# Kernel tuning notes

Hardware: AMD Instinct MI355X
Metric: run time of the kernel (lower is better)

The kernel has to match this reference:

```python
import jax, jax.numpy as jnp
import numpy as np

B, S, H, L, OUT = 16, 64, 512, 2, 10  # batch, seq, hidden(=input_dim), num_layers, output_dim
NSTEP, TSTEP = 2, 4
L2 = L * L  # stacked LSTM layers per level_step


def setup_inputs() -> dict:
    key = jax.random.key(0)
    ks = jax.random.split(key, 24)
    s = 1.0 / np.sqrt(H)
    inp = {
        "x": jax.random.normal(ks[0], (B, S, H), jnp.float32),
        "Wp_in": jax.random.normal(ks[1], (H, H), jnp.float32) * s,
        "bp_in": jnp.zeros((H,), jnp.float32),
        "low_Wih": jax.random.normal(ks[2], (L2, 4 * H, H), jnp.float32) * s,
        "low_Whh": jax.random.normal(ks[3], (L2, 4 * H, H), jnp.float32) * s,
        "low_bih": jax.random.normal(ks[4], (L2, 4 * H), jnp.float32) * s,
        "low_bhh": jax.random.normal(ks[5], (L2, 4 * H), jnp.float32) * s,
        "high_Wih": jax.random.normal(ks[6], (L2, 4 * H, H), jnp.float32) * s,
        "high_Whh": jax.random.normal(ks[7], (L2, 4 * H, H), jnp.float32) * s,
        "high_bih": jax.random.normal(ks[8], (L2, 4 * H), jnp.float32) * s,
        "high_bhh": jax.random.normal(ks[9], (L2, 4 * H), jnp.float32) * s,
        "W_lowproj": jax.random.normal(ks[10], (H, H), jnp.float32) * s,
        "W_highproj": jax.random.normal(ks[11], (H, H), jnp.float32) * s,
        "ln_g": jnp.ones((2 * H,), jnp.float32),
        "ln_b": jnp.zeros((2 * H,), jnp.float32),
        "W1": jax.random.normal(ks[12], (H, 2 * H), jnp.float32) * (1.0 / np.sqrt(2 * H)),
        "b1": jnp.zeros((H,), jnp.float32),
        "W2": jax.random.normal(ks[13], (H // 2, H), jnp.float32) * s,
        "b2": jnp.zeros((H // 2,), jnp.float32),
        "W3": jax.random.normal(ks[14], (OUT, H // 2), jnp.float32) * (1.0 / np.sqrt(H // 2)),
        "b3": jnp.zeros((OUT,), jnp.float32),
    }
    return inp


def _lstm_layer(x, Wih, Whh, bih, bhh):
    # x: (B, S, H) -> (B, S, H), PyTorch LSTM gate order i,f,g,o, zero init state
    b, _, h = x.shape
    h0 = jnp.zeros((b, h), x.dtype)
    bias = bih + bhh

    def step(carry, xt):
        hp, cp = carry
        g = xt @ Wih.T + hp @ Whh.T + bias
        i, f, gg, o = jnp.split(g, 4, axis=-1)
        c = jax.nn.sigmoid(f) * cp + jax.nn.sigmoid(i) * jnp.tanh(gg)
        hn = jax.nn.sigmoid(o) * jnp.tanh(c)
        return (hn, c), hn

    _, ys = jax.lax.scan(step, (h0, h0), jnp.swapaxes(x, 0, 1))
    return jnp.swapaxes(ys, 0, 1)


def _run_net(x, Wih, Whh, bih, bhh):
    for l in range(Wih.shape[0]):
        x = _lstm_layer(x, Wih[l], Whh[l], bih[l], bhh[l])
    return x


def _level_step(first, second, emb, Wih, Whh, bih, bhh, Wproj):
    combined = first + second @ Wproj.T + emb  # broadcast (B,1,H)+(B,S,H)
    return _run_net(combined, Wih, Whh, bih, bhh)


def reference(x, Wp_in, bp_in, low_Wih, low_Whh, low_bih, low_bhh,
              high_Wih, high_Whh, high_bih, high_bhh,
              W_lowproj, W_highproj, ln_g, ln_b, W1, b1, W2, b2, W3, b3):
    emb = x @ Wp_in.T + bp_in  # (B, S, H)
    low = jnp.zeros((x.shape[0], 1, H), x.dtype)
    high = jnp.zeros((x.shape[0], 1, H), x.dtype)
    total = NSTEP * TSTEP
    for step in range(total - 1):
        low = _level_step(low, high, emb, low_Wih, low_Whh, low_bih, low_bhh, W_lowproj)
        if (step + 1) % TSTEP == 0:
            high = _level_step(high, low, emb, high_Wih, high_Whh, high_bih, high_bhh, W_highproj)
    low = jax.lax.stop_gradient(low)   # torch.no_grad over the loop
    high = jax.lax.stop_gradient(high)
    low = _level_step(low, high, emb, low_Wih, low_Whh, low_bih, low_bhh, W_lowproj)
    high = _level_step(high, low, emb, high_Wih, high_Whh, high_bih, high_bhh, W_highproj)
    combined = jnp.concatenate([low, high], axis=-1)  # (B, S, 2H)
    mu = combined.mean(-1, keepdims=True)
    var = combined.var(-1, keepdims=True)
    normed = (combined - mu) / jnp.sqrt(var + 1e-5) * ln_g + ln_b
    h1 = jax.nn.relu(normed @ W1.T + b1)
    h2 = jax.nn.relu(h1 @ W2.T + b2)
    return h2 @ W3.T + b3  # (B, S, OUT)
```

## Files before the change

### kernel.cpp

```cpp
#include <hip/hip_runtime.h>

#define BB 16
#define SS 64
#define HH 512
#define MR (BB*SS)
#define GN (4*HH)
#define NLAYER 4
#define OUTD 10
#define LBLK 32
#define NSLOT (3*SS + 2)

typedef float   floatx4  __attribute__((ext_vector_type(4)));
typedef __bf16  bf16x8   __attribute__((ext_vector_type(8)));
typedef unsigned short ushort8v __attribute__((ext_vector_type(8)));
typedef int     intx4    __attribute__((ext_vector_type(4)));

#define MFMA_BF16(a,b,c) __builtin_amdgcn_mfma_f32_16x16x32_bf16((a),(b),(c),0,0,0)

static __device__ __forceinline__ unsigned short f2bf_rne(float f) {
  union { float f; unsigned u; } v; v.f = f;
  unsigned r = v.u + 0x7fffu + ((v.u >> 16) & 1u);
  return (unsigned short)(r >> 16);
}

static __device__ __forceinline__ bf16x8 load_a8(const float* __restrict__ p) {
  float4 x0 = *(const float4*)p;
  float4 x1 = *(const float4*)(p + 4);
  union { ushort8v u; bf16x8 b; } c;
  c.u[0] = f2bf_rne(x0.x); c.u[1] = f2bf_rne(x0.y);
  c.u[2] = f2bf_rne(x0.z); c.u[3] = f2bf_rne(x0.w);
  c.u[4] = f2bf_rne(x1.x); c.u[5] = f2bf_rne(x1.y);
  c.u[6] = f2bf_rne(x1.z); c.u[7] = f2bf_rne(x1.w);
  return c.b;
}

static __device__ __forceinline__ float sigm(float x) {
  return __builtin_amdgcn_rcpf(1.f + __expf(-x));
}
static __device__ __forceinline__ float tanh_fast(float x) {
  return 1.f - 2.f * __builtin_amdgcn_rcpf(1.f + __expf(2.f * x));
}

static __device__ __forceinline__ intx4 coh_load16(const void* p) {
  intx4 r;
  asm volatile("global_load_dwordx4 %0, %1, off sc0 sc1"
               : "=v"(r) : "v"(p) : "memory");
  return r;
}
static __device__ __forceinline__ void coh_store_dword(void* p, unsigned v) {
  asm volatile("global_store_dword %0, %1, off sc0 sc1"
               :: "v"(p), "v"(v) : "memory");
}
static __device__ __forceinline__ void wait_vm0() {
  asm volatile("s_waitcnt vmcnt(0)" ::: "memory");
}

__global__ void hrm_zero_f32(float* p, int n) {
  int i = blockIdx.x * 256 + threadIdx.x;
  if (i < n) p[i] = 0.f;
}
__global__ void hrm_zero_u16(unsigned short* p, int n) {
  int i = blockIdx.x * 256 + threadIdx.x;
  if (i < n) p[i] = 0;
}
__global__ void hrm_cvt_bf16(unsigned short* __restrict__ dst,
                             const float* __restrict__ src, int n) {
  int i = blockIdx.x * 256 + threadIdx.x;
  if (i < n) dst[i] = f2bf_rne(src[i]);
}
__global__ void hrm_addvec(float* __restrict__ o, const float* __restrict__ a,
                           const float* __restrict__ b, int n) {
  int i = blockIdx.x * 256 + threadIdx.x;
  if (i < n) o[i] = a[i] + b[i];
}

__global__ __launch_bounds__(64) void hrm_gemm16(
    const float* __restrict__ A, const unsigned short* __restrict__ W,
    float* __restrict__ C, const float* __restrict__ bias0,
    const float* __restrict__ bias1, const float* __restrict__ res0,
    const float* __restrict__ res1, int N, int K, int relu, int out_bf16)
{
  const int lane  = threadIdx.x;
  const int mrow  = lane & 15;
  const int kq    = lane >> 4;
  const int m_base = blockIdx.y << 4;
  const int n_base = blockIdx.x << 6;

  floatx4 acc[4] = {{0.f,0.f,0.f,0.f},{0.f,0.f,0.f,0.f},
                    {0.f,0.f,0.f,0.f},{0.f,0.f,0.f,0.f}};
  const float* ap = A + (size_t)(m_base + mrow) * K + kq * 8;
  const unsigned short* wp = W + (size_t)(n_base + mrow) * K + kq * 8;

  #pragma unroll 4
  for (int kt = 0; kt < K; kt += 32) {
    bf16x8 a = load_a8(ap + kt);
    #pragma unroll
    for (int sub = 0; sub < 4; ++sub) {
      bf16x8 b = *(const bf16x8*)(wp + (size_t)sub * 16 * K + kt);
      acc[sub] = MFMA_BF16(a, b, acc[sub]);
    }
  }
  #pragma unroll
  for (int sub = 0; sub < 4; ++sub) {
    int n = n_base + sub * 16 + mrow;
    if (n < N) {
      #pragma unroll
      for (int r = 0; r < 4; ++r) {
        int m = m_base + kq * 4 + r;
        size_t idx = (size_t)m * N + n;
        float v = acc[sub][r];
        if (bias0) v += bias0[n];
        if (bias1) v += bias1[n];
        if (res0)  v += res0[idx];
        if (res1)  v += res1[idx];
        if (relu)  v = fmaxf(v, 0.f);
        if (out_bf16) ((unsigned short*)C)[idx] = f2bf_rne(v);
        else          C[idx] = v;
      }
    }
  }
}

__global__ __launch_bounds__(256, 1) void hrm_stack(
    const unsigned short* __restrict__ xin,
    const unsigned short* __restrict__ Wih,
    const unsigned short* __restrict__ Whh,
    const float* __restrict__ bsum,
    float* __restrict__ Y,
    int* __restrict__ hb,
    int sibase)
{
  __shared__ unsigned short hs_x[BB][520];
  __shared__ unsigned short hs_h[BB][520];
  __shared__ float gt[4][BB][16];
  __shared__ float cst[BB][16];

  const int tid  = threadIdx.x;
  const int bid  = blockIdx.x;
  const int l    = bid >> 5;
  const int sub  = bid & 31;
  const int lane = tid & 63;
  const int w    = tid >> 6;
  const int mrow = lane & 15;
  const int kq   = lane >> 4;
  const int b    = tid >> 4;
  const int j0   = tid & 15;

  cst[b][j0] = 0.f;

  bf16x8 wif[16], whf[16];
  {
    const size_t rowoff = (size_t)(w * HH + sub * 16 + mrow) * HH + kq * 8;
    const unsigned short* p = Wih + (size_t)l * GN * HH + rowoff;
    const unsigned short* q = Whh + (size_t)l * GN * HH + rowoff;
    #pragma unroll
    for (int kt = 0; kt < 16; ++kt) {
      wif[kt] = *(const bf16x8*)(p + kt * 32);
      whf[kt] = *(const bf16x8*)(q + kt * 32);
    }
  }
  float bias_v[4];
  #pragma unroll
  for (int w2 = 0; w2 < 4; ++w2)
    bias_v[w2] = bsum[l * GN + w2 * HH + sub * 16 + j0];

  int* myhb = hb + (size_t)l * SS * BB * HH;
  const bool needx = (l > 0);
  const int* xhb = needx ? (hb + (size_t)(l - 1) * SS * BB * HH) : hb;

  int spin_budget = 1 << 17;

  for (int t = 0; t < SS; ++t) {
    const bool needh = (t > 0);
    const int wr_slot = (l == 3) ? (t & 1) : t;

    bf16x8 ax0[16];
    if (l == 0) {
      const unsigned short* xr = xin + (size_t)(mrow * SS + t) * HH + kq * 8;
      #pragma unroll
      for (int kt = 0; kt < 16; ++kt) ax0[kt] = *(const bf16x8*)(xr + kt * 32);
    }

    if (needx || needh) {
      const unsigned xtag = (unsigned)(sibase + t + 1);
      const unsigned htag = (unsigned)(sibase + t);
      const int rd_slot = (l == 3) ? ((t - 1) & 1) : (t - 1);
      const int* xp = xhb + (size_t)t * BB * HH + tid * 32;
      const int* hp = myhb + (size_t)rd_slot * BB * HH + tid * 32;
      intx4 sx[8], sh[8];
      int fails = 0;
      for (;;) {
        if (needx) {
          #pragma unroll
          for (int k = 0; k < 8; ++k) sx[k] = coh_load16(xp + k * 4);
        }
        if (needh) {
          #pragma unroll
          for (int k = 0; k < 8; ++k) sh[k] = coh_load16(hp + k * 4);
        }
        wait_vm0();
        __builtin_amdgcn_sched_barrier(0);
        unsigned bad = 0;
        if (needx) {
          #pragma unroll
          for (int k = 0; k < 8; ++k)
            #pragma unroll
            for (int i = 0; i < 4; ++i)
              bad |= ((unsigned)sx[k][i] >> 16) ^ xtag;
        }
        if (needh) {
          #pragma unroll
          for (int k = 0; k < 8; ++k)
            #pragma unroll
            for (int i = 0; i < 4; ++i)
              bad |= ((unsigned)sh[k][i] >> 16) ^ htag;
        }
        if (bad == 0) break;
        if (--spin_budget < 0) break;
        if (++fails > 16) __builtin_amdgcn_s_sleep(8);
      }
      const int srow  = tid >> 4;
      const int scol0 = (tid & 15) * 32;
      if (needx) {
        #pragma unroll
        for (int k = 0; k < 8; k += 2) {
          intx4 lo = sx[k], hi = sx[k + 1], pk;
          pk[0] = (lo[0] & 0xffff) | (lo[1] << 16);
          pk[1] = (lo[2] & 0xffff) | (lo[3] << 16);
          pk[2] = (hi[0] & 0xffff) | (hi[1] << 16);
          pk[3] = (hi[2] & 0xffff) | (hi[3] << 16);
          *(intx4*)&hs_x[srow][scol0 + k * 4] = pk;
        }
      }
      if (needh) {
        #pragma unroll
        for (int k = 0; k < 8; k += 2) {
          intx4 lo = sh[k], hi = sh[k + 1], pk;
          pk[0] = (lo[0] & 0xffff) | (lo[1] << 16);
          pk[1] = (lo[2] & 0xffff) | (lo[3] << 16);
          pk[2] = (hi[0] & 0xffff) | (hi[1] << 16);
          pk[3] = (hi[2] & 0xffff) | (hi[3] << 16);
          *(intx4*)&hs_h[srow][scol0 + k * 4] = pk;
        }
      }
    }
    __syncthreads();

    floatx4 accx = {0.f,0.f,0.f,0.f}, acch = {0.f,0.f,0.f,0.f};
    if (l == 0) {
      #pragma unroll
      for (int kt = 0; kt < 16; ++kt) accx = MFMA_BF16(ax0[kt], wif[kt], accx);
    } else {
      const unsigned short* xr = &hs_x[mrow][kq * 8];
      #pragma unroll
      for (int kt = 0; kt < 16; ++kt) {
        bf16x8 a = *(const bf16x8*)(xr + kt * 32);
        accx = MFMA_BF16(a, wif[kt], accx);
      }
    }
    if (needh) {
      const unsigned short* hr = &hs_h[mrow][kq * 8];
      #pragma unroll
      for (int kt = 0; kt < 16; ++kt) {
        bf16x8 a = *(const bf16x8*)(hr + kt * 32);
        acch = MFMA_BF16(a, whf[kt], acch);
      }
    }
    floatx4 a0 = accx + acch;
    #pragma unroll
    for (int r = 0; r < 4; ++r) gt[w][kq * 4 + r][mrow] = a0[r];
    __syncthreads();

    const unsigned tag = (unsigned)(sibase + t + 1) << 16;
    int* hb_cur = myhb + (size_t)wr_slot * BB * HH;
    {
      int n = sub * 16 + j0;
      float gi = gt[0][b][j0] + bias_v[0];
      float gf = gt[1][b][j0] + bias_v[1];
      float gg = gt[2][b][j0] + bias_v[2];
      float go = gt[3][b][j0] + bias_v[3];
      float ig = sigm(gi), fg = sigm(gf), gvv = tanh_fast(gg), og = sigm(go);
      float c = fg * cst[b][j0] + ig * gvv;
      cst[b][j0] = c;
      float h = og * tanh_fast(c);
      coh_store_dword(hb_cur + b * HH + n, tag | (unsigned)f2bf_rne(h));
      if (l == 3) Y[(size_t)(b * SS + t) * HH + n] = h;
    }
  }
}

__global__ __launch_bounds__(256) void hrm_ln(
    const float* __restrict__ low, const float* __restrict__ high,
    const float* __restrict__ g, const float* __restrict__ bta,
    float* __restrict__ out)
{
  __shared__ float sa[256], sb[256];
  const int row = blockIdx.x;
  const int tid = threadIdx.x;
  float vals[4], s = 0.f, s2 = 0.f;
  #pragma unroll
  for (int i = 0; i < 4; ++i) {
    int c = tid + i * 256;
    float v = (c < HH) ? low[(size_t)row * HH + c]
                       : high[(size_t)row * HH + (c - HH)];
    vals[i] = v; s += v; s2 += v * v;
  }
  sa[tid] = s; sb[tid] = s2; __syncthreads();
  for (int off = 128; off > 0; off >>= 1) {
    if (tid < off) { sa[tid] += sa[tid + off]; sb[tid] += sb[tid + off]; }
    __syncthreads();
  }
  float mu  = sa[0] * (1.f / 1024.f);
  float var = sb[0] * (1.f / 1024.f) - mu * mu;
  float rstd = rsqrtf(var + 1e-5f);
  #pragma unroll
  for (int i = 0; i < 4; ++i) {
    int c = tid + i * 256;
    out[(size_t)row * 1024 + c] = (vals[i] - mu) * rstd * g[c] + bta[c];
  }
}

extern "C" void kernel_launch(void* const* d_in, const int* in_sizes, int n_in,
                              void* d_out, int out_size, void* d_ws, size_t ws_size,
                              hipStream_t stream) {
  const float* x        = (const float*)d_in[0];
  const float* Wp_in    = (const float*)d_in[1];
  const float* bp_in    = (const float*)d_in[2];
  const float* low_Wih  = (const float*)d_in[3];
  const float* low_Whh  = (const float*)d_in[4];
  const float* low_bih  = (const float*)d_in[5];
  const float* low_bhh  = (const float*)d_in[6];
  const float* high_Wih = (const float*)d_in[7];
  const float* high_Whh = (const float*)d_in[8];
  const float* high_bih = (const float*)d_in[9];
  const float* high_bhh = (const float*)d_in[10];
  const float* W_lowp   = (const float*)d_in[11];
  const float* W_highp  = (const float*)d_in[12];
  const float* ln_g     = (const float*)d_in[13];
  const float* ln_b     = (const float*)d_in[14];
  const float* W1       = (const float*)d_in[15];
  const float* b1       = (const float*)d_in[16];
  const float* W2       = (const float*)d_in[17];
  const float* b2       = (const float*)d_in[18];
  const float* W3       = (const float*)d_in[19];
  const float* b3       = (const float*)d_in[20];

  char* wsp = (char*)d_ws;
  size_t off = 0;
  auto alloc = [&](size_t bytes) -> void* {
    void* p = wsp + off;
    off += (bytes + 255) & ~(size_t)255;
    return p;
  };
  const size_t WSZ = (size_t)GN * HH;
  unsigned short* wp_b   = (unsigned short*)alloc(512u * 512u * 2);
  unsigned short* lwih_b = (unsigned short*)alloc(NLAYER * WSZ * 2);
  unsigned short* lwhh_b = (unsigned short*)alloc(NLAYER * WSZ * 2);
  unsigned short* hwih_b = (unsigned short*)alloc(NLAYER * WSZ * 2);
  unsigned short* hwhh_b = (unsigned short*)alloc(NLAYER * WSZ * 2);
  unsigned short* wlp_b  = (unsigned short*)alloc(512u * 512u * 2);
  unsigned short* whp_b  = (unsigned short*)alloc(512u * 512u * 2);
  unsigned short* w1_b   = (unsigned short*)alloc(512u * 1024u * 2);
  unsigned short* w2_b   = (unsigned short*)alloc(256u * 512u * 2);
  unsigned short* w3p_b  = (unsigned short*)alloc(64u * 256u * 2);

  float* bsum_l = (float*)alloc(NLAYER * GN * 4);
  float* bsum_h = (float*)alloc(NLAYER * GN * 4);

  float* emb    = (float*)alloc((size_t)MR * HH * 4);
  float* lowb   = (float*)alloc((size_t)MR * HH * 4);
  float* highb  = (float*)alloc((size_t)MR * HH * 4);
  float* xa     = (float*)alloc((size_t)MR * HH * 4);
  float* xb     = (float*)alloc((size_t)MR * HH * 4);
  int* hbuf = (int*)alloc((size_t)NSLOT * BB * HH * 4);
  unsigned short* comb = (unsigned short*)xa;
  float* normed = (float*)hbuf;

  auto cvt = [&](unsigned short* dst, const float* src, int n) {
    hrm_cvt_bf16<<<(n + 255) / 256, 256, 0, stream>>>(dst, src, n);
  };
  cvt(wp_b,   Wp_in,    512 * 512);
  cvt(lwih_b, low_Wih,  (int)(NLAYER * WSZ));
  cvt(lwhh_b, low_Whh,  (int)(NLAYER * WSZ));
  cvt(hwih_b, high_Wih, (int)(NLAYER * WSZ));
  cvt(hwhh_b, high_Whh, (int)(NLAYER * WSZ));
  cvt(wlp_b,  W_lowp,   512 * 512);
  cvt(whp_b,  W_highp,  512 * 512);
  cvt(w1_b,   W1,       512 * 1024);
  cvt(w2_b,   W2,       256 * 512);
  hrm_zero_u16<<<(64 * 256 + 255) / 256, 256, 0, stream>>>(w3p_b, 64 * 256);
  cvt(w3p_b, W3, OUTD * 256);

  hrm_addvec<<<(NLAYER * GN + 255) / 256, 256, 0, stream>>>(
      bsum_l, low_bih, low_bhh, NLAYER * GN);
  hrm_addvec<<<(NLAYER * GN + 255) / 256, 256, 0, stream>>>(
      bsum_h, high_bih, high_bhh, NLAYER * GN);

  hrm_zero_f32<<<(MR * HH + 255) / 256, 256, 0, stream>>>(lowb,  MR * HH);
  hrm_zero_f32<<<(MR * HH + 255) / 256, 256, 0, stream>>>(highb, MR * HH);
  hrm_zero_f32<<<(NSLOT * BB * HH + 255) / 256, 256, 0, stream>>>(
      (float*)hbuf, NSLOT * BB * HH);

  hrm_gemm16<<<dim3(HH / 64, MR / 16), 64, 0, stream>>>(
      x, wp_b, emb, bp_in, nullptr, nullptr, nullptr, HH, HH, 0, 0);

  const int seq[10] = {0, 0, 0, 0, 1, 0, 0, 0, 0, 1};
  for (int si = 0; si < 10; ++si) {
    const bool hi = seq[si] != 0;
    float* target = hi ? highb : lowb;
    const float* first  = target;
    const float* second = hi ? lowb : highb;
    const unsigned short* proj = hi ? whp_b : wlp_b;

    hrm_gemm16<<<dim3(HH / 64, MR / 16), 64, 0, stream>>>(
        second, proj, (float*)comb, nullptr, nullptr, first, emb, HH, HH, 0, 1);

    hrm_stack<<<NLAYER * LBLK, 256, 0, stream>>>(
        comb, hi ? hwih_b : lwih_b, hi ? hwhh_b : lwhh_b,
        hi ? bsum_h : bsum_l, target, hbuf, si * 64);
  }

  hrm_ln<<<MR, 256, 0, stream>>>(lowb, highb, ln_g, ln_b, normed);
  hrm_gemm16<<<dim3(HH / 64, MR / 16), 64, 0, stream>>>(
      normed, w1_b, xa, b1, nullptr, nullptr, nullptr, HH, 2 * HH, 1, 0);
  hrm_gemm16<<<dim3(256 / 64, MR / 16), 64, 0, stream>>>(
      xa, w2_b, xb, b2, nullptr, nullptr, nullptr, 256, HH, 1, 0);
  hrm_gemm16<<<dim3(1, MR / 16), 64, 0, stream>>>(
      xb, w3p_b, (float*)d_out, b3, nullptr, nullptr, nullptr, OUTD, 256, 0, 0);
  (void)in_sizes; (void)n_in; (void)out_size; (void)ws_size;
}
```

Before: 3.654 ms.

## Halve LSTM stack blocks per layer, each block computing 32 hidden units

The persistent wavefront-pipelined LSTM kernel now uses 16 blocks per layer instead of 32. Each block keeps two 16-column weight slices in registers and computes 32 hidden units per step. Fewer blocks means fewer participants in each cross-block h handoff and less redundant staging of the shared x/h rows into LDS. In exchange, each block runs twice the MFMA work per step and holds twice the weight registers, which may cause register spills.

```diff
diff --git a/kernel.cpp b/kernel.cpp
--- a/kernel.cpp
+++ b/kernel.cpp
@@ -7,7 +7,7 @@
 #define GN (4*HH)
 #define NLAYER 4
 #define OUTD 10
-#define LBLK 32
+#define LBLK 16
 #define NSLOT (3*SS + 2)
 
 typedef float   floatx4  __attribute__((ext_vector_type(4)));
@@ -132,13 +132,13 @@
 {
   __shared__ unsigned short hs_x[BB][520];
   __shared__ unsigned short hs_h[BB][520];
-  __shared__ float gt[4][BB][16];
-  __shared__ float cst[BB][16];
+  __shared__ float gt[4][BB][32];
+  __shared__ float cst[BB][32];
 
   const int tid  = threadIdx.x;
   const int bid  = blockIdx.x;
-  const int l    = bid >> 5;
-  const int sub  = bid & 31;
+  const int l    = bid >> 4;
+  const int sub  = bid & 15;
   const int lane = tid & 63;
   const int w    = tid >> 6;
   const int mrow = lane & 15;
@@ -146,23 +146,27 @@
   const int b    = tid >> 4;
   const int j0   = tid & 15;
 
-  cst[b][j0] = 0.f;
-
-  bf16x8 wif[16], whf[16];
+  cst[b][j0] = 0.f; cst[b][j0 + 16] = 0.f;
+
+  bf16x8 wif[2][16], whf[2][16];
   {
-    const size_t rowoff = (size_t)(w * HH + sub * 16 + mrow) * HH + kq * 8;
+    const size_t rowoff = (size_t)(w * HH + sub * 32 + mrow) * HH + kq * 8;
     const unsigned short* p = Wih + (size_t)l * GN * HH + rowoff;
     const unsigned short* q = Whh + (size_t)l * GN * HH + rowoff;
     #pragma unroll
     for (int kt = 0; kt < 16; ++kt) {
-      wif[kt] = *(const bf16x8*)(p + kt * 32);
-      whf[kt] = *(const bf16x8*)(q + kt * 32);
-    }
-  }
-  float bias_v[4];
+      wif[0][kt] = *(const bf16x8*)(p + kt * 32);
+      wif[1][kt] = *(const bf16x8*)(p + (size_t)16 * HH + kt * 32);
+      whf[0][kt] = *(const bf16x8*)(q + kt * 32);
+      whf[1][kt] = *(const bf16x8*)(q + (size_t)16 * HH + kt * 32);
+    }
+  }
+  float bias_v[2][4];
   #pragma unroll
-  for (int w2 = 0; w2 < 4; ++w2)
-    bias_v[w2] = bsum[l * GN + w2 * HH + sub * 16 + j0];
+  for (int qq = 0; qq < 2; ++qq)
+    #pragma unroll
+    for (int w2 = 0; w2 < 4; ++w2)
+      bias_v[qq][w2] = bsum[l * GN + w2 * HH + sub * 32 + j0 + qq * 16];
 
   int* myhb = hb + (size_t)l * SS * BB * HH;
   const bool needx = (l > 0);
@@ -246,16 +250,20 @@
     }
     __syncthreads();
 
-    floatx4 accx = {0.f,0.f,0.f,0.f}, acch = {0.f,0.f,0.f,0.f};
+    floatx4 a0 = {0.f,0.f,0.f,0.f}, a1 = {0.f,0.f,0.f,0.f};
     if (l == 0) {
       #pragma unroll
-      for (int kt = 0; kt < 16; ++kt) accx = MFMA_BF16(ax0[kt], wif[kt], accx);
+      for (int kt = 0; kt < 16; ++kt) {
+        a0 = MFMA_BF16(ax0[kt], wif[0][kt], a0);
+        a1 = MFMA_BF16(ax0[kt], wif[1][kt], a1);
+      }
     } else {
       const unsigned short* xr = &hs_x[mrow][kq * 8];
       #pragma unroll
       for (int kt = 0; kt < 16; ++kt) {
         bf16x8 a = *(const bf16x8*)(xr + kt * 32);
-        accx = MFMA_BF16(a, wif[kt], accx);
+        a0 = MFMA_BF16(a, wif[0][kt], a0);
+        a1 = MFMA_BF16(a, wif[1][kt], a1);
       }
     }
     if (needh) {
@@ -263,25 +271,30 @@
       #pragma unroll
       for (int kt = 0; kt < 16; ++kt) {
         bf16x8 a = *(const bf16x8*)(hr + kt * 32);
-        acch = MFMA_BF16(a, whf[kt], acch);
-      }
-    }
-    floatx4 a0 = accx + acch;
+        a0 = MFMA_BF16(a, whf[0][kt], a0);
+        a1 = MFMA_BF16(a, whf[1][kt], a1);
+      }
+    }
     #pragma unroll
-    for (int r = 0; r < 4; ++r) gt[w][kq * 4 + r][mrow] = a0[r];
+    for (int r = 0; r < 4; ++r) {
+      gt[w][kq * 4 + r][mrow]      = a0[r];
+      gt[w][kq * 4 + r][16 + mrow] = a1[r];
+    }
     __syncthreads();
 
     const unsigned tag = (unsigned)(sibase + t + 1) << 16;
     int* hb_cur = myhb + (size_t)wr_slot * BB * HH;
-    {
-      int n = sub * 16 + j0;
-      float gi = gt[0][b][j0] + bias_v[0];
-      float gf = gt[1][b][j0] + bias_v[1];
-      float gg = gt[2][b][j0] + bias_v[2];
-      float go = gt[3][b][j0] + bias_v[3];
+    #pragma unroll
+    for (int q = 0; q < 2; ++q) {
+      int jj = j0 + q * 16;
+      int n  = sub * 32 + jj;
+      float gi = gt[0][b][jj] + bias_v[q][0];
+      float gf = gt[1][b][jj] + bias_v[q][1];
+      float gg = gt[2][b][jj] + bias_v[q][2];
+      float go = gt[3][b][jj] + bias_v[q][3];
       float ig = sigm(gi), fg = sigm(gf), gvv = tanh_fast(gg), og = sigm(go);
-      float c = fg * cst[b][j0] + ig * gvv;
-      cst[b][j0] = c;
+      float c = fg * cst[b][jj] + ig * gvv;
+      cst[b][jj] = c;
       float h = og * tanh_fast(c);
       coh_store_dword(hb_cur + b * HH + n, tag | (unsigned)f2bf_rne(h));
       if (l == 3) Y[(size_t)(b * SS + t) * HH + n] = h;
```

Result: slower. 4.014 ms (+9.8%).

## Fuse next-step projection GEMM into LSTM stack kernel tail via tagged ring buffer

Applied to the files above, without the earlier changes.

The per-level-step projection GEMM (second-state times projection weight, plus residual and embedding) now runs at the end of the recurrent stack kernel, so it no longer needs its own launch. It reads the freshly produced top-layer hidden states straight from a ring buffer, enlarged to a full sequence per layer, by polling per-element tags. Carried level states are kept as bf16 copies, and fp32 outputs are written only on the final two steps. This removes ten separate GEMM launches and the serialization between them and the stack kernels. In exchange it adds spin-waiting in the tail and uses bf16 rather than fp32 for the residual term.

```diff
diff --git a/kernel.cpp b/kernel.cpp
--- a/kernel.cpp
+++ b/kernel.cpp
@@ -8,7 +8,7 @@
 #define NLAYER 4
 #define OUTD 10
 #define LBLK 32
-#define NSLOT (3*SS + 2)
+#define NSLOT (4*SS)
 
 typedef float   floatx4  __attribute__((ext_vector_type(4)));
 typedef __bf16  bf16x8   __attribute__((ext_vector_type(8)));
@@ -21,6 +21,9 @@
   union { float f; unsigned u; } v; v.f = f;
   unsigned r = v.u + 0x7fffu + ((v.u >> 16) & 1u);
   return (unsigned short)(r >> 16);
+}
+static __device__ __forceinline__ float bf2f(unsigned w) {
+  union { unsigned u; float f; } c; c.u = w << 16; return c.f;
 }
 
 static __device__ __forceinline__ bf16x8 load_a8(const float* __restrict__ p) {
@@ -44,6 +47,12 @@
 static __device__ __forceinline__ intx4 coh_load16(const void* p) {
   intx4 r;
   asm volatile("global_load_dwordx4 %0, %1, off sc0 sc1"
+               : "=v"(r) : "v"(p) : "memory");
+  return r;
+}
+static __device__ __forceinline__ unsigned coh_load4(const void* p) {
+  unsigned r;
+  asm volatile("global_load_dword %0, %1, off sc0 sc1"
                : "=v"(r) : "v"(p) : "memory");
   return r;
 }
@@ -127,8 +136,14 @@
     const unsigned short* __restrict__ Whh,
     const float* __restrict__ bsum,
     float* __restrict__ Y,
+    unsigned short* __restrict__ state16,
     int* __restrict__ hb,
-    int sibase)
+    int sibase,
+    const unsigned short* __restrict__ projw,
+    const unsigned short* __restrict__ tfirst,
+    const unsigned short* __restrict__ tsecond,
+    const float* __restrict__ emb,
+    unsigned short* __restrict__ comb_out)
 {
   __shared__ unsigned short hs_x[BB][520];
   __shared__ unsigned short hs_h[BB][520];
@@ -172,7 +187,6 @@
 
   for (int t = 0; t < SS; ++t) {
     const bool needh = (t > 0);
-    const int wr_slot = (l == 3) ? (t & 1) : t;
 
     bf16x8 ax0[16];
     if (l == 0) {
@@ -181,67 +195,68 @@
       for (int kt = 0; kt < 16; ++kt) ax0[kt] = *(const bf16x8*)(xr + kt * 32);
     }
 
-    if (needx || needh) {
+    const int srow  = tid >> 4;
+    const int scol0 = (tid & 15) * 32;
+
+    if (needx) {
       const unsigned xtag = (unsigned)(sibase + t + 1);
-      const unsigned htag = (unsigned)(sibase + t);
-      const int rd_slot = (l == 3) ? ((t - 1) & 1) : (t - 1);
       const int* xp = xhb + (size_t)t * BB * HH + tid * 32;
-      const int* hp = myhb + (size_t)rd_slot * BB * HH + tid * 32;
-      intx4 sx[8], sh[8];
+      intx4 sx[8];
       int fails = 0;
       for (;;) {
-        if (needx) {
-          #pragma unroll
-          for (int k = 0; k < 8; ++k) sx[k] = coh_load16(xp + k * 4);
-        }
-        if (needh) {
-          #pragma unroll
-          for (int k = 0; k < 8; ++k) sh[k] = coh_load16(hp + k * 4);
-        }
+        #pragma unroll
+        for (int k = 0; k < 8; ++k) sx[k] = coh_load16(xp + k * 4);
         wait_vm0();
         __builtin_amdgcn_sched_barrier(0);
         unsigned bad = 0;
-        if (needx) {
+        #pragma unroll
+        for (int k = 0; k < 8; ++k)
           #pragma unroll
-          for (int k = 0; k < 8; ++k)
-            #pragma unroll
-            for (int i = 0; i < 4; ++i)
-              bad |= ((unsigned)sx[k][i] >> 16) ^ xtag;
-        }
-        if (needh) {
-          #pragma unroll
-          for (int k = 0; k < 8; ++k)
-            #pragma unroll
-            for (int i = 0; i < 4; ++i)
-              bad |= ((unsigned)sh[k][i] >> 16) ^ htag;
-        }
+          for (int i = 0; i < 4; ++i)
+            bad |= ((unsigned)sx[k][i] >> 16) ^ xtag;
         if (bad == 0) break;
         if (--spin_budget < 0) break;
         if (++fails > 16) __builtin_amdgcn_s_sleep(8);
       }
-      const int srow  = tid >> 4;
-      const int scol0 = (tid & 15) * 32;
-      if (needx) {
+      #pragma unroll
+      for (int k = 0; k < 8; k += 2) {
+        intx4 lo = sx[k], hi = sx[k + 1], pk;
+        pk[0] = (lo[0] & 0xffff) | (lo[1] << 16);
+        pk[1] = (lo[2] & 0xffff) | (lo[3] << 16);
+        pk[2] = (hi[0] & 0xffff) | (hi[1] << 16);
+        pk[3] = (hi[2] & 0xffff) | (hi[3] << 16);
+        *(intx4*)&hs_x[srow][scol0 + k * 4] = pk;
+      }
+    }
+
+    if (needh) {
+      const unsigned htag = (unsigned)(sibase + t);
+      const int* hp = myhb + (size_t)(t - 1) * BB * HH + tid * 32;
+      intx4 sh[8];
+      int fails = 0;
+      for (;;) {
         #pragma unroll
-        for (int k = 0; k < 8; k += 2) {
-          intx4 lo = sx[k], hi = sx[k + 1], pk;
-          pk[0] = (lo[0] & 0xffff) | (lo[1] << 16);
-          pk[1] = (lo[2] & 0xffff) | (lo[3] << 16);
-          pk[2] = (hi[0] & 0xffff) | (hi[1] << 16);
-          pk[3] = (hi[2] & 0xffff) | (hi[3] << 16);
-          *(intx4*)&hs_x[srow][scol0 + k * 4] = pk;
-        }
-      }
-      if (needh) {
+        for (int k = 0; k < 8; ++k) sh[k] = coh_load16(hp + k * 4);
+        wait_vm0();
+        __builtin_amdgcn_sched_barrier(0);
+        unsigned bad = 0;
         #pragma unroll
-        for (int k = 0; k < 8; k += 2) {
-          intx4 lo = sh[k], hi = sh[k + 1], pk;
-          pk[0] = (lo[0] & 0xffff) | (lo[1] << 16);
-          pk[1] = (lo[2] & 0xffff) | (lo[3] << 16);
-          pk[2] = (hi[0] & 0xffff) | (hi[1] << 16);
-          pk[3] = (hi[2] & 0xffff) | (hi[3] << 16);
-          *(intx4*)&hs_h[srow][scol0 + k * 4] = pk;
-        }
+        for (int k = 0; k < 8; ++k)
+          #pragma unroll
+          for (int i = 0; i < 4; ++i)
+            bad |= ((unsigned)sh[k][i] >> 16) ^ htag;
+        if (bad == 0) break;
+        if (--spin_budget < 0) break;
+        if (++fails > 16) __builtin_amdgcn_s_sleep(8);
+      }
+      #pragma unroll
+      for (int k = 0; k < 8; k += 2) {
+        intx4 lo = sh[k], hi = sh[k + 1], pk;
+        pk[0] = (lo[0] & 0xffff) | (lo[1] << 16);
+        pk[1] = (lo[2] & 0xffff) | (lo[3] << 16);
+        pk[2] = (hi[0] & 0xffff) | (hi[1] << 16);
+        pk[3] = (hi[2] & 0xffff) | (hi[3] << 16);
+        *(intx4*)&hs_h[srow][scol0 + k * 4] = pk;
       }
     }
     __syncthreads();
@@ -272,7 +287,7 @@
     __syncthreads();
 
     const unsigned tag = (unsigned)(sibase + t + 1) << 16;
-    int* hb_cur = myhb + (size_t)wr_slot * BB * HH;
+    int* hb_cur = myhb + (size_t)t * BB * HH;
     {
       int n = sub * 16 + j0;
       float gi = gt[0][b][j0] + bias_v[0];
@@ -284,7 +299,87 @@
       cst[b][j0] = c;
       float h = og * tanh_fast(c);
       coh_store_dword(hb_cur + b * HH + n, tag | (unsigned)f2bf_rne(h));
-      if (l == 3) Y[(size_t)(b * SS + t) * HH + n] = h;
+      if (l == 3) {
+        size_t idx = (size_t)(b * SS + t) * HH + n;
+        state16[idx] = f2bf_rne(h);
+        if (Y) Y[idx] = h;
+      }
+    }
+  }
+
+  if (comb_out) {
+    const int* ring3 = hb + (size_t)3 * SS * BB * HH;
+    const int job    = bid * 4 + w;
+    const int m_base = (job >> 3) << 4;
+    const int n_base = (job & 7) << 6;
+
+    const int arow = m_base + mrow;
+    const int ab   = arow >> 6, at = arow & 63;
+    const unsigned atag = (unsigned)(sibase + at + 1);
+    const int* aring = ring3 + ((size_t)at * BB + ab) * HH;
+
+    floatx4 acc[4] = {{0.f,0.f,0.f,0.f},{0.f,0.f,0.f,0.f},
+                      {0.f,0.f,0.f,0.f},{0.f,0.f,0.f,0.f}};
+    const unsigned short* wp = projw + (size_t)(n_base + mrow) * HH + kq * 8;
+
+    for (int kt = 0; kt < HH; kt += 32) {
+      const int col = kq * 8 + kt;
+      bf16x8 a;
+      if (!tsecond) {
+        const int* p = aring + col;
+        for (;;) {
+          intx4 lo = coh_load16(p);
+          intx4 hi = coh_load16(p + 4);
+          wait_vm0();
+          __builtin_amdgcn_sched_barrier(0);
+          unsigned bad = 0;
+          #pragma unroll
+          for (int i = 0; i < 4; ++i)
+            bad |= (((unsigned)lo[i] >> 16) ^ atag) |
+                   (((unsigned)hi[i] >> 16) ^ atag);
+          if (bad == 0 || --spin_budget < 0) {
+            union { ushort8v u; bf16x8 bb; } c;
+            #pragma unroll
+            for (int i = 0; i < 4; ++i) {
+              c.u[i]     = (unsigned short)lo[i];
+              c.u[4 + i] = (unsigned short)hi[i];
+            }
+            a = c.bb;
+            break;
+          }
+        }
+      } else {
+        a = *(const bf16x8*)(tsecond + (size_t)arow * HH + col);
+      }
+      #pragma unroll
+      for (int s2 = 0; s2 < 4; ++s2) {
+        bf16x8 bfr = *(const bf16x8*)(wp + (size_t)s2 * 16 * HH + kt);
+        acc[s2] = MFMA_BF16(a, bfr, acc[s2]);
+      }
+    }
+    #pragma unroll
+    for (int s2 = 0; s2 < 4; ++s2) {
+      int n = n_base + s2 * 16 + mrow;
+      #pragma unroll
+      for (int r = 0; r < 4; ++r) {
+        int m = m_base + kq * 4 + r;
+        size_t idx = (size_t)m * HH + n;
+        float v = acc[s2][r] + emb[idx];
+        if (!tfirst) {
+          const int mt = m & 63, mb = m >> 6;
+          const int* fp_ = ring3 + ((size_t)mt * BB + mb) * HH + n;
+          const unsigned ftag = (unsigned)(sibase + mt + 1);
+          for (;;) {
+            unsigned fw = coh_load4(fp_);
+            wait_vm0();
+            __builtin_amdgcn_sched_barrier(0);
+            if ((fw >> 16) == ftag || --spin_budget < 0) { v += bf2f(fw & 0xffff); break; }
+          }
+        } else {
+          v += bf2f(tfirst[idx]);
+        }
+        comb_out[idx] = f2bf_rne(v);
+      }
     }
   }
 }
@@ -370,11 +465,13 @@
   float* emb    = (float*)alloc((size_t)MR * HH * 4);
   float* lowb   = (float*)alloc((size_t)MR * HH * 4);
   float* highb  = (float*)alloc((size_t)MR * HH * 4);
-  float* xa     = (float*)alloc((size_t)MR * HH * 4);
-  float* xb     = (float*)alloc((size_t)MR * HH * 4);
+  unsigned short* comb   = (unsigned short*)alloc((size_t)MR * HH * 2);
+  unsigned short* low16  = (unsigned short*)alloc((size_t)MR * HH * 2);
+  unsigned short* high16 = (unsigned short*)alloc((size_t)MR * HH * 2);
   int* hbuf = (int*)alloc((size_t)NSLOT * BB * HH * 4);
-  unsigned short* comb = (unsigned short*)xa;
   float* normed = (float*)hbuf;
+  float* xa     = (float*)comb;
+  float* xb     = (float*)high16;
 
   auto cvt = [&](unsigned short* dst, const float* src, int n) {
     hrm_cvt_bf16<<<(n + 255) / 256, 256, 0, stream>>>(dst, src, n);
@@ -396,28 +493,36 @@
   hrm_addvec<<<(NLAYER * GN + 255) / 256, 256, 0, stream>>>(
       bsum_h, high_bih, high_bhh, NLAYER * GN);
 
-  hrm_zero_f32<<<(MR * HH + 255) / 256, 256, 0, stream>>>(lowb,  MR * HH);
-  hrm_zero_f32<<<(MR * HH + 255) / 256, 256, 0, stream>>>(highb, MR * HH);
   hrm_zero_f32<<<(NSLOT * BB * HH + 255) / 256, 256, 0, stream>>>(
       (float*)hbuf, NSLOT * BB * HH);
+  hrm_zero_u16<<<(MR * HH + 255) / 256, 256, 0, stream>>>(low16,  MR * HH);
+  hrm_zero_u16<<<(MR * HH + 255) / 256, 256, 0, stream>>>(high16, MR * HH);
 
   hrm_gemm16<<<dim3(HH / 64, MR / 16), 64, 0, stream>>>(
       x, wp_b, emb, bp_in, nullptr, nullptr, nullptr, HH, HH, 0, 0);
+  cvt(comb, emb, MR * HH);
 
   const int seq[10] = {0, 0, 0, 0, 1, 0, 0, 0, 0, 1};
   for (int si = 0; si < 10; ++si) {
-    const bool hi = seq[si] != 0;
-    float* target = hi ? highb : lowb;
-    const float* first  = target;
-    const float* second = hi ? lowb : highb;
-    const unsigned short* proj = hi ? whp_b : wlp_b;
-
-    hrm_gemm16<<<dim3(HH / 64, MR / 16), 64, 0, stream>>>(
-        second, proj, (float*)comb, nullptr, nullptr, first, emb, HH, HH, 0, 1);
-
+    const int ty = seq[si];
+    float* Yp = (si == 8) ? lowb : (si == 9) ? highb : nullptr;
+    unsigned short* st16 = ty ? high16 : low16;
+
+    const unsigned short* projw = nullptr;
+    const unsigned short* tfirst = nullptr;
+    const unsigned short* tsecond = nullptr;
+    unsigned short* comb_out = nullptr;
+    if (si < 9) {
+      const int t2 = seq[si + 1];
+      projw = t2 ? whp_b : wlp_b;
+      if (t2 != ty)        tfirst  = t2 ? high16 : low16;
+      if ((t2 ^ 1) != ty)  tsecond = t2 ? low16 : high16;
+      comb_out = comb;
+    }
     hrm_stack<<<NLAYER * LBLK, 256, 0, stream>>>(
-        comb, hi ? hwih_b : lwih_b, hi ? hwhh_b : lwhh_b,
-        hi ? bsum_h : bsum_l, target, hbuf, si * 64);
+        comb, ty ? hwih_b : lwih_b, ty ? hwhh_b : lwhh_b,
+        ty ? bsum_h : bsum_l, Yp, st16, hbuf, si * 64,
+        projw, tfirst, tsecond, emb, comb_out);
   }
 
   hrm_ln<<<MR, 256, 0, stream>>>(lowb, highb, ln_g, ln_b, normed);
```

Measured after the change: 3.575 ms. 1.02x faster.
